# Kernel optimization log

Measured on AMD Instinct MI355X. Metric: run time of the kernel, lower is better.

## Reference

```python
import jax, jax.numpy as jnp
import numpy as np

K = 5       # local window size (odd)
G = 4       # groups

def _gconv1x1(x, w):
    # grouped 1x1 conv: x (b,c,h,w), w (g, c_out_g, c_in_g) -> (b,g,c_out_g,h,w)
    b, c, h, wd = x.shape
    g, co, ci = w.shape
    xg = x.reshape(b, g, ci, h, wd)
    return jnp.einsum('bgihw,goi->bgohw', xg, w)

def _windows(f, h, w):
    # f: (b,g,n,h+2p,w+2p) -> (b,g,n,h,w,K*K), row-major over (ki,kj)
    # matches torch .unfold(2,K,1).unfold(3,K,1).view(..., -1)
    return jnp.stack([f[..., i:i + h, j:j + w]
                      for i in range(K) for j in range(K)], axis=-1)

def setup_inputs() -> dict:
    key = jax.random.key(0)
    k1, k2, k3, k4 = jax.random.split(key, 4)
    x = jax.random.normal(k1, (2, 128, 96, 96), dtype=jnp.float32)
    wq = jax.random.normal(k2, (G, 32, 32), dtype=jnp.float32) * 0.1
    wk = jax.random.normal(k3, (G, 32, 32), dtype=jnp.float32) * 0.1
    wv = jax.random.normal(k4, (G, 32, 32), dtype=jnp.float32) * 0.1
    return {"x": x, "wq": wq, "wk": wk, "wv": wv}

def reference(x, wq, wk, wv):
    b, c, h, w = x.shape
    p = K // 2
    # query: plain grouped 1x1 conv, broadcast over window dim
    q = _gconv1x1(x, wq)[..., None]                      # (b,g,n,h,w,1)
    # key/value: reflect-pad (1x1 conv commutes with padding, same as torch's
    # Conv2d(..., padding=k//2, padding_mode='reflect'))
    xp = jnp.pad(x, ((0, 0), (0, 0), (p, p), (p, p)), mode='reflect')
    kf = _gconv1x1(xp, wk)                               # (b,g,n,h+2p,w+2p)
    vf = _gconv1x1(xp, wv)
    kwin = _windows(kf, h, w)                            # (b,g,n,h,w,K*K)
    vwin = _windows(vf, h, w)
    attn = jax.nn.softmax(q * kwin, axis=-1)             # per-channel window softmax
    y = (attn * vwin).sum(-1)                            # (b,g,n,h,w)
    return y.reshape(b, -1, h, w)                        # (b, c_out, h, w)
```

## Files before the change

kernel.cpp:

```cpp
#include <hip/hip_runtime.h>


#define HW 96
#define RG 12
#define NPOS 144
#define CSTR 36

typedef _Float16 half8  __attribute__((ext_vector_type(8)));
typedef _Float16 half2v __attribute__((ext_vector_type(2)));
typedef float    float4v __attribute__((ext_vector_type(4)));
typedef unsigned int uint4v __attribute__((ext_vector_type(4)));

__device__ __forceinline__ int refl(int i) {
    i = (i < 0) ? -i : i;
    i = (i > 95) ? (190 - i) : i;
    return i;
}

__global__ __launch_bounds__(256) void fused_attn(
    const float* __restrict__ x, const float* __restrict__ wq,
    const float* __restrict__ wk, const float* __restrict__ wv,
    float* __restrict__ out)
{
    __shared__ alignas(16) unsigned char smem[9216 + 20736];
    _Float16*     xs  = (_Float16*)smem;
    unsigned int* kvb = (unsigned int*)(smem + 9216);
    _Float16*     qs  = (_Float16*)smem;

    const int tid = threadIdx.x;
    const int g = blockIdx.y, b = blockIdx.z;
    const int h0 = (blockIdx.x / 12) * 8;
    const int w0 = (blockIdx.x % 12) * 8;
    const float* xg = x + (size_t)(b * 128 + g * 32) * (HW * HW);

    const int wA   = min(max(w0 - 4, 0), 80);
    const int colB = wA - w0 + 2;
    #pragma unroll
    for (int it = 0; it < 6; it++) {
        int idx = it * 256 + tid;
        int seg = idx & 3;
        int pr  = idx >> 2;
        int ch  = pr & 31;
        int row = pr >> 5;
        int iy  = refl(h0 + row - 2);
        const float4v f4 = *(const float4v*)(xg + ch * (HW * HW) + iy * HW + wA + seg * 4);
        int col0 = colB + seg * 4;
        #pragma unroll
        for (int e = 0; e < 4; e++) {
            int col = col0 + e;
            if (col >= 0 && col < RG)
                xs[(row * RG + col) * 32 + ch] = (_Float16)f4[e];
        }
    }

    const int wid  = tid >> 6;
    const int lane = tid & 63;
    const int n0   = wid * 8;
    const int col  = lane & 15;
    const int quad = lane >> 4;
    const int koff = quad * 8;

    const float* wrow = (col < 8) ? (wk + (g * 32 + n0 + col) * 32)
                                  : (wv + (g * 32 + n0 + col - 8) * 32);
    half8 bkv;
    #pragma unroll
    for (int j = 0; j < 8; j++)
        bkv[j] = (_Float16)wrow[koff + j];

    half8 bq = {0, 0, 0, 0, 0, 0, 0, 0};
    if (col < 8) {
        const float* qr = wq + (g * 32 + n0 + col) * 32;
        #pragma unroll
        for (int j = 0; j < 8; j++)
            bq[j] = (_Float16)(qr[koff + j] * 1.44269504f);
    }

    if (w0 == 0 || w0 == 88) {
        __syncthreads();
        const int left = (w0 == 0);
        for (int it = 0; it < 3; it++) {
            int idx = it * 256 + tid;
            int ch  = idx & 31;
            int rr  = idx >> 5;
            int row = rr >> 1, wc = rr & 1;
            int dstc = left ? wc : (10 + wc);
            int srcc = left ? (4 - wc) : (8 - wc);
            xs[(row * RG + dstc) * 32 + ch] = xs[(row * RG + srcc) * 32 + ch];
        }
    }
    __syncthreads();

    _Float16* kv16 = (_Float16*)kvb;
    #pragma unroll
    for (int t = 0; t < 9; t++) {
        int pa = t * 16 + col;
        half8 a = *(const half8*)&xs[pa * 32 + koff];
        float4v d = {0.f, 0.f, 0.f, 0.f};
        d = __builtin_amdgcn_mfma_f32_16x16x32_f16(a, bkv, d, 0, 0, 0);
        int c    = n0 + (col & 7);
        int half_ = col >> 3;
        #pragma unroll
        for (int r = 0; r < 4; r++) {
            int p = t * 16 + quad * 4 + r;
            kv16[(p * CSTR + c) * 2 + half_] = (_Float16)d[r];
        }
    }

    float4v dqv[4];
    #pragma unroll
    for (int t = 0; t < 4; t++) {
        int mp = t * 16 + col;
        int p  = ((mp >> 3) + 2) * RG + (mp & 7) + 2;
        half8 a = *(const half8*)&xs[p * 32 + koff];
        float4v z = {0.f, 0.f, 0.f, 0.f};
        dqv[t] = __builtin_amdgcn_mfma_f32_16x16x32_f16(a, bq, z, 0, 0, 0);
    }

    __syncthreads();

    if (col < 8) {
        #pragma unroll
        for (int t = 0; t < 4; t++) {
            #pragma unroll
            for (int r = 0; r < 4; r++) {
                int pix = t * 16 + quad * 4 + r;
                qs[pix * 32 + n0 + col] = (_Float16)dqv[t][r];
            }
        }
    }
    __syncthreads();

    const int ty = lane >> 3, tx = lane & 7;

    half8 qh = *(const half8*)&qs[lane * 32 + n0];
    float qf[8];
    #pragma unroll
    for (int c = 0; c < 8; c++) qf[c] = (float)qh[c];

    float den[8], num[8];
    #pragma unroll
    for (int c = 0; c < 8; c++) { den[c] = 0.f; num[c] = 0.f; }

    #pragma unroll
    for (int dy = 0; dy < 5; dy++) {
        const unsigned int* base = &kvb[((ty + dy) * RG + tx) * CSTR + n0];
        uint4v t0[5], t1[5];
        #pragma unroll
        for (int dx = 0; dx < 5; dx++) {
            t0[dx] = *(const uint4v*)(base + dx * CSTR);
            t1[dx] = *(const uint4v*)(base + dx * CSTR + 4);
        }
        #pragma unroll
        for (int dx = 0; dx < 5; dx++) {
            #pragma unroll
            for (int c = 0; c < 8; c++) {
                unsigned int u = (c < 4) ? t0[dx][c] : t1[dx][c - 4];
                half2v kv = __builtin_bit_cast(half2v, u);
                float e = __builtin_amdgcn_exp2f(qf[c] * (float)kv[0]);
                den[c] += e;
                num[c] = fmaf(e, (float)kv[1], num[c]);
            }
        }
    }

    float* outp = out + (size_t)((b * 128 + g * 32 + n0) * HW + (h0 + ty)) * HW + (w0 + tx);
    #pragma unroll
    for (int c = 0; c < 8; c++)
        outp[c * (HW * HW)] = num[c] * __builtin_amdgcn_rcpf(den[c]);
}

extern "C" void kernel_launch(void* const* d_in, const int* in_sizes, int n_in,
                              void* d_out, int out_size, void* d_ws, size_t ws_size,
                              hipStream_t stream) {
    const float* x  = (const float*)d_in[0];
    const float* wq = (const float*)d_in[1];
    const float* wk = (const float*)d_in[2];
    const float* wv = (const float*)d_in[3];
    float* out = (float*)d_out;

    dim3 grid(144, 4, 2);
    fused_attn<<<grid, 256, 0, stream>>>(x, wq, wk, wv, out);
}
```

Measured before the change: 91.77 us.

## Split fused kernel into separate QKV projection and window-attention kernels

Splits the single fused kernel into two. The first computes the q/k/v 1x1 projections once per pixel into fp16 channel-last workspace buffers. The second loads k/v tiles (with halo) and q from the workspace, interleaves k and v into shared memory, and runs the windowed softmax. This removes the fused kernel's redundant halo projection (144 positions computed per 64 output pixels) and its shared-memory x staging, at the cost of a second launch and extra global traffic through the workspace.

Result: no change. 90.55 us (-1.3%).

```diff
diff --git a/kernel.cpp b/kernel.cpp
--- a/kernel.cpp
+++ b/kernel.cpp
@@ -3,8 +3,8 @@
 
 #define HW 96
 #define RG 12
-#define NPOS 144
 #define CSTR 36
+#define PXN 9216
 
 typedef _Float16 half8  __attribute__((ext_vector_type(8)));
 typedef _Float16 half2v __attribute__((ext_vector_type(2)));
@@ -17,122 +17,107 @@
     return i;
 }
 
-__global__ __launch_bounds__(256) void fused_attn(
+__global__ __launch_bounds__(256) void conv_qkv(
     const float* __restrict__ x, const float* __restrict__ wq,
     const float* __restrict__ wk, const float* __restrict__ wv,
-    float* __restrict__ out)
+    _Float16* __restrict__ qp, _Float16* __restrict__ kp, _Float16* __restrict__ vp)
 {
-    __shared__ alignas(16) unsigned char smem[9216 + 20736];
-    _Float16*     xs  = (_Float16*)smem;
-    unsigned int* kvb = (unsigned int*)(smem + 9216);
-    _Float16*     qs  = (_Float16*)smem;
+    const int tid  = threadIdx.x;
+    const int g = blockIdx.y, b = blockIdx.z;
+    const int lane = tid & 63, wid = tid >> 6;
+    const int col  = lane & 15;
+    const int quad = lane >> 4;
+    const int koff = quad * 8;
+    const int pxw  = blockIdx.x * 128 + wid * 32;
+    const float* xg = x + (size_t)(b * 128 + g * 32) * PXN;
+    const size_t plane = (size_t)(b * 4 + g) * PXN * 32;
+
+    const float* wsrc[3] = {wq, wk, wv};
+    half8 frag[6];
+    #pragma unroll
+    for (int T = 0; T < 6; T++) {
+        const float* wr = wsrc[T >> 1] + (g * 32 + (T & 1) * 16 + col) * 32 + koff;
+        float sc = (T < 2) ? 1.44269504f : 1.0f;
+        #pragma unroll
+        for (int j = 0; j < 8; j++) frag[T][j] = (_Float16)(wr[j] * sc);
+    }
+
+    _Float16* outp[3] = {qp, kp, vp};
+    #pragma unroll
+    for (int s = 0; s < 2; s++) {
+        int apx = pxw + s * 16 + col;
+        half8 a;
+        #pragma unroll
+        for (int j = 0; j < 8; j++)
+            a[j] = (_Float16)xg[(koff + j) * PXN + apx];
+        #pragma unroll
+        for (int T = 0; T < 6; T++) {
+            float4v d = {0.f, 0.f, 0.f, 0.f};
+            d = __builtin_amdgcn_mfma_f32_16x16x32_f16(a, frag[T], d, 0, 0, 0);
+            _Float16* pl = outp[T >> 1];
+            #pragma unroll
+            for (int r = 0; r < 4; r++) {
+                int dpx = pxw + s * 16 + quad * 4 + r;
+                pl[plane + (size_t)dpx * 32 + (T & 1) * 16 + col] = (_Float16)d[r];
+            }
+        }
+    }
+}
+
+__global__ __launch_bounds__(256) void attn(
+    const _Float16* __restrict__ qp, const _Float16* __restrict__ kp,
+    const _Float16* __restrict__ vp, float* __restrict__ out)
+{
+    __shared__ unsigned int kvb[144 * CSTR];
 
     const int tid = threadIdx.x;
     const int g = blockIdx.y, b = blockIdx.z;
     const int h0 = (blockIdx.x / 12) * 8;
     const int w0 = (blockIdx.x % 12) * 8;
-    const float* xg = x + (size_t)(b * 128 + g * 32) * (HW * HW);
+    const int lane = tid & 63, wid = tid >> 6, n0 = wid * 8;
+    const int ty = lane >> 3, tx = lane & 7;
+    const size_t plane = (size_t)(b * 4 + g) * PXN * 32;
 
-    const int wA   = min(max(w0 - 4, 0), 80);
-    const int colB = wA - w0 + 2;
+    const int qpx = (h0 + ty) * HW + (w0 + tx);
+    uint4v qu = *(const uint4v*)(qp + plane + (size_t)qpx * 32 + n0);
+
+    const int wA  = min(max(w0 - 4, 0), 80);
+    const int off = w0 - 2 - wA;
     #pragma unroll
-    for (int it = 0; it < 6; it++) {
-        int idx = it * 256 + tid;
-        int seg = idx & 3;
-        int pr  = idx >> 2;
-        int ch  = pr & 31;
-        int row = pr >> 5;
-        int iy  = refl(h0 + row - 2);
-        const float4v f4 = *(const float4v*)(xg + ch * (HW * HW) + iy * HW + wA + seg * 4);
-        int col0 = colB + seg * 4;
-        #pragma unroll
-        for (int e = 0; e < 4; e++) {
-            int col = col0 + e;
-            if (col >= 0 && col < RG)
-                xs[(row * RG + col) * 32 + ch] = (_Float16)f4[e];
-        }
-    }
-
-    const int wid  = tid >> 6;
-    const int lane = tid & 63;
-    const int n0   = wid * 8;
-    const int col  = lane & 15;
-    const int quad = lane >> 4;
-    const int koff = quad * 8;
-
-    const float* wrow = (col < 8) ? (wk + (g * 32 + n0 + col) * 32)
-                                  : (wv + (g * 32 + n0 + col - 8) * 32);
-    half8 bkv;
-    #pragma unroll
-    for (int j = 0; j < 8; j++)
-        bkv[j] = (_Float16)wrow[koff + j];
-
-    half8 bq = {0, 0, 0, 0, 0, 0, 0, 0};
-    if (col < 8) {
-        const float* qr = wq + (g * 32 + n0 + col) * 32;
-        #pragma unroll
-        for (int j = 0; j < 8; j++)
-            bq[j] = (_Float16)(qr[koff + j] * 1.44269504f);
-    }
-
-    if (w0 == 0 || w0 == 88) {
-        __syncthreads();
-        const int left = (w0 == 0);
-        for (int it = 0; it < 3; it++) {
-            int idx = it * 256 + tid;
-            int ch  = idx & 31;
-            int rr  = idx >> 5;
-            int row = rr >> 1, wc = rr & 1;
-            int dstc = left ? wc : (10 + wc);
-            int srcc = left ? (4 - wc) : (8 - wc);
-            xs[(row * RG + dstc) * 32 + ch] = xs[(row * RG + srcc) * 32 + ch];
-        }
-    }
-    __syncthreads();
-
-    _Float16* kv16 = (_Float16*)kvb;
-    #pragma unroll
-    for (int t = 0; t < 9; t++) {
-        int pa = t * 16 + col;
-        half8 a = *(const half8*)&xs[pa * 32 + koff];
-        float4v d = {0.f, 0.f, 0.f, 0.f};
-        d = __builtin_amdgcn_mfma_f32_16x16x32_f16(a, bkv, d, 0, 0, 0);
-        int c    = n0 + (col & 7);
-        int half_ = col >> 3;
-        #pragma unroll
-        for (int r = 0; r < 4; r++) {
-            int p = t * 16 + quad * 4 + r;
-            kv16[(p * CSTR + c) * 2 + half_] = (_Float16)d[r];
-        }
-    }
-
-    float4v dqv[4];
-    #pragma unroll
-    for (int t = 0; t < 4; t++) {
-        int mp = t * 16 + col;
-        int p  = ((mp >> 3) + 2) * RG + (mp & 7) + 2;
-        half8 a = *(const half8*)&xs[p * 32 + koff];
-        float4v z = {0.f, 0.f, 0.f, 0.f};
-        dqv[t] = __builtin_amdgcn_mfma_f32_16x16x32_f16(a, bq, z, 0, 0, 0);
-    }
-
-    __syncthreads();
-
-    if (col < 8) {
-        #pragma unroll
-        for (int t = 0; t < 4; t++) {
+    for (int it = 0; it < 3; it++) {
+        int idx  = it * 256 + tid;
+        int chunk = idx & 3, px_i = (idx >> 2) & 15, row = idx >> 6;
+        int iy = refl(h0 + row - 2);
+        size_t gaddr = plane + (size_t)(iy * HW + wA + px_i) * 32 + chunk * 8;
+        uint4v kq = *(const uint4v*)(kp + gaddr);
+        uint4v vq = *(const uint4v*)(vp + gaddr);
+        int s = px_i - off;
+        if (s >= 0 && s < RG) {
+            int base = (row * RG + s) * CSTR + chunk * 8;
             #pragma unroll
-            for (int r = 0; r < 4; r++) {
-                int pix = t * 16 + quad * 4 + r;
-                qs[pix * 32 + n0 + col] = (_Float16)dqv[t][r];
+            for (int e = 0; e < 4; e++) {
+                kvb[base + 2 * e]     = __builtin_amdgcn_perm(vq[e], kq[e], 0x05040100);
+                kvb[base + 2 * e + 1] = __builtin_amdgcn_perm(vq[e], kq[e], 0x07060302);
             }
         }
     }
     __syncthreads();
 
-    const int ty = lane >> 3, tx = lane & 7;
+    if (off != 2) {
+        const int left = (w0 == 0);
+        #pragma unroll
+        for (int it = 0; it < 3; it++) {
+            int idx = it * 256 + tid;
+            int ch = idx & 31, rr = idx >> 5;
+            int row = rr >> 1, wc = rr & 1;
+            int dst = left ? wc : (10 + wc);
+            int src = left ? (4 - wc) : (8 - wc);
+            kvb[(row * RG + dst) * CSTR + ch] = kvb[(row * RG + src) * CSTR + ch];
+        }
+        __syncthreads();
+    }
 
-    half8 qh = *(const half8*)&qs[lane * 32 + n0];
+    half8 qh = __builtin_bit_cast(half8, qu);
     float qf[8];
     #pragma unroll
     for (int c = 0; c < 8; c++) qf[c] = (float)qh[c];
@@ -178,6 +163,11 @@
     const float* wv = (const float*)d_in[3];
     float* out = (float*)d_out;
 
-    dim3 grid(144, 4, 2);
-    fused_attn<<<grid, 256, 0, stream>>>(x, wq, wk, wv, out);
+    const size_t PLSZ = (size_t)2 * 4 * PXN * 32;
+    _Float16* qp = (_Float16*)d_ws;
+    _Float16* kp = qp + PLSZ;
+    _Float16* vp = kp + PLSZ;
+
+    conv_qkv<<<dim3(72, 4, 2), 256, 0, stream>>>(x, wq, wk, wv, qp, kp, vp);
+    attn<<<dim3(144, 4, 2), 256, 0, stream>>>(qp, kp, vp, out);
 }
```
